# Kernel tuning notes

Measured on AMD Instinct MI355X. Metric: run time of the kernel, lower is better.

Reference implementation:

```python
import jax, jax.numpy as jnp
import numpy as np

N_NODES = 50000
N_EDGES = 1600000
N_GRAPHS = 64
F_IN = 256
H = 1024
EPS = 1e-5


def setup_inputs() -> dict:
    key = jax.random.key(0)
    ks = jax.random.split(key, 6)
    x = jax.random.normal(ks[0], (N_NODES, F_IN), dtype=jnp.float32)
    edge_index = jax.random.randint(ks[1], (2, N_EDGES), 0, N_NODES, dtype=jnp.int32)
    batch = jnp.sort(jax.random.randint(ks[2], (N_NODES,), 0, N_GRAPHS, dtype=jnp.int32))
    # Glorot-ish init for GCN weights
    W0 = jax.random.normal(ks[3], (F_IN, H), dtype=jnp.float32) * (1.0 / np.sqrt(F_IN))
    b0 = jnp.zeros((H,), dtype=jnp.float32)
    Ws = jax.random.normal(ks[4], (3, H, H), dtype=jnp.float32) * (1.0 / np.sqrt(H))
    bs = jnp.zeros((3, H), dtype=jnp.float32)
    gammas = jnp.ones((4, H), dtype=jnp.float32)
    betas = jnp.zeros((4, H), dtype=jnp.float32)
    return {"x": x, "edge_index": edge_index, "batch": batch,
            "W0": W0, "b0": b0, "Ws": Ws, "bs": bs,
            "gammas": gammas, "betas": betas}


def _gcn_norm(edge_index, n_nodes):
    # Add self-loops (PyG GCNConv default), compute symmetric normalization.
    loops = jnp.arange(n_nodes, dtype=edge_index.dtype)
    row = jnp.concatenate([edge_index[0], loops])  # sources
    col = jnp.concatenate([edge_index[1], loops])  # targets (aggregation index)
    ones = jnp.ones(row.shape[0], dtype=jnp.float32)
    deg = jax.ops.segment_sum(ones, col, num_segments=n_nodes)
    dinv = jnp.where(deg > 0, jax.lax.rsqrt(deg), 0.0)
    norm = dinv[row] * dinv[col]  # [E + N]
    return row, col, norm


def _layer(h, W, b, gamma, beta, row, col, norm):
    ht = h @ W                                           # [N, H] GEMM
    msg = ht[row] * norm[:, None]                        # gather + scale
    agg = jax.ops.segment_sum(msg, col, num_segments=N_NODES) + b
    mu = jnp.mean(agg, axis=-1, keepdims=True)
    var = jnp.mean(jnp.square(agg - mu), axis=-1, keepdims=True)
    hn = (agg - mu) * jax.lax.rsqrt(var + EPS) * gamma + beta
    return jax.nn.relu(hn)


def reference(x, edge_index, batch, W0, b0, Ws, bs, gammas, betas):
    row, col, norm = _gcn_norm(edge_index, N_NODES)
    h = _layer(x, W0, b0, gammas[0], betas[0], row, col, norm)
    for i in range(3):
        h = _layer(h, Ws[i], bs[i], gammas[i + 1], betas[i + 1], row, col, norm)
    # scatter_mean over batch (graph-level pooling)
    sums = jax.ops.segment_sum(h, batch, num_segments=N_GRAPHS)
    cnt = jax.ops.segment_sum(jnp.ones((N_NODES,), jnp.float32), batch, num_segments=N_GRAPHS)
    return sums / jnp.maximum(cnt, 1.0)[:, None]
```

## Files before the change

### kernel.cpp

```cpp
#include <hip/hip_runtime.h>
#include <hip/hip_bf16.h>
#include <stdint.h>

#define NN 50000
#define NE 1600000
#define NG 64
#define FIN 256
#define HD 1024
#define EPSV 1e-5f

typedef __bf16 bf16;
typedef float f32x4 __attribute__((ext_vector_type(4)));
typedef int i32x4 __attribute__((ext_vector_type(4)));

typedef const __attribute__((address_space(1))) void* gptr_as1;
typedef __attribute__((address_space(3))) void* lptr_as3;

__device__ __forceinline__ void load_g2l_16(const void* g, const void* l) {
  __builtin_amdgcn_global_load_lds((gptr_as1)(uintptr_t)g,
                                   (lptr_as3)(uint32_t)(uintptr_t)l, 16, 0, 0);
}

__global__ void hist_kernel(const int* __restrict__ col, int* __restrict__ cnt, int E) {
  int e = blockIdx.x * 256 + threadIdx.x;
  if (e < E) atomicAdd(&cnt[col[e]], 1);
}

__global__ void scan_partial_kernel(const int* __restrict__ cnt, int* __restrict__ partial, int n) {
  __shared__ int red[4];
  int i = blockIdx.x * 256 + threadIdx.x;
  int v = (i < n) ? cnt[i] : 0;
  #pragma unroll
  for (int off = 32; off; off >>= 1) v += __shfl_down(v, off, 64);
  if ((threadIdx.x & 63) == 0) red[threadIdx.x >> 6] = v;
  __syncthreads();
  if (threadIdx.x == 0) partial[blockIdx.x] = red[0] + red[1] + red[2] + red[3];
}

__global__ void scan_scan_kernel(int* __restrict__ partial, int nb) {
  __shared__ int s[256];
  int t = threadIdx.x;
  int v = (t < nb) ? partial[t] : 0;
  s[t] = v;
  __syncthreads();
  for (int off = 1; off < 256; off <<= 1) {
    int x = (t >= off) ? s[t - off] : 0;
    __syncthreads();
    s[t] += x;
    __syncthreads();
  }
  if (t < nb) partial[t] = s[t] - v;
}

__global__ void scan_final_kernel(const int* __restrict__ cnt, const int* __restrict__ partial,
                                  int* __restrict__ row_ptr, float* __restrict__ dinv,
                                  int n, int E) {
  __shared__ int s[256];
  int t = threadIdx.x;
  int i = blockIdx.x * 256 + t;
  int v = (i < n) ? cnt[i] : 0;
  s[t] = v;
  __syncthreads();
  for (int off = 1; off < 256; off <<= 1) {
    int x = (t >= off) ? s[t - off] : 0;
    __syncthreads();
    s[t] += x;
    __syncthreads();
  }
  if (i < n) {
    row_ptr[i] = partial[blockIdx.x] + s[t] - v;
    dinv[i] = rsqrtf((float)(v + 1));
  }
  if (i == 0) row_ptr[n] = E;
}

__global__ void scatter_kernel(const int* __restrict__ rowi, const int* __restrict__ coli,
                               const int* __restrict__ row_ptr, int* __restrict__ fill,
                               const float* __restrict__ dinv,
                               int2* __restrict__ csr_sw, int E) {
  int e = blockIdx.x * 256 + threadIdx.x;
  if (e >= E) return;
  int s = rowi[e], d = coli[e];
  int pos = row_ptr[d] + atomicAdd(&fill[d], 1);
  int2 p;
  p.x = s;
  p.y = __float_as_int(dinv[s] * dinv[d]);
  csr_sw[pos] = p;
}

__global__ __launch_bounds__(256) void quant_x_kernel(const float* __restrict__ x,
                                                      uint8_t* __restrict__ X8,
                                                      float* __restrict__ xscale) {
  int row = blockIdx.x * 4 + (threadIdx.x >> 6);
  int t = threadIdx.x & 63;
  float4 v = ((const float4*)(x + (size_t)row * FIN))[t];
  float m = fmaxf(fmaxf(fabsf(v.x), fabsf(v.y)), fmaxf(fabsf(v.z), fabsf(v.w)));
  #pragma unroll
  for (int off = 32; off; off >>= 1) m = fmaxf(m, __shfl_xor(m, off, 64));
  float inv = (m > 0.f) ? 127.0f / m : 0.f;
  int q0 = min(127, max(-127, __float2int_rn(v.x * inv))) + 128;
  int q1 = min(127, max(-127, __float2int_rn(v.y * inv))) + 128;
  int q2 = min(127, max(-127, __float2int_rn(v.z * inv))) + 128;
  int q3 = min(127, max(-127, __float2int_rn(v.w * inv))) + 128;
  uint32_t p = ((uint32_t)q0) | ((uint32_t)q1 << 8) |
               ((uint32_t)q2 << 16) | ((uint32_t)q3 << 24);
  ((uint32_t*)X8)[(size_t)row * 64 + t] = p;
  if (t == 0) xscale[row] = (m > 0.f) ? m / 127.0f : 0.f;
}

__global__ __launch_bounds__(256) void agg0_kernel(
    const uint8_t* __restrict__ X8, const float* __restrict__ xscale,
    const int* __restrict__ row_ptr, const int2* __restrict__ csr_sw,
    const float* __restrict__ dinv,
    int8_t* __restrict__ AX8, float* __restrict__ axscale) {
  const int node = blockIdx.x * 4 + (threadIdx.x >> 6);
  const int t = threadIdx.x & 63;

  float acc[4] = {};
  float sw = 0.f;

  float dn = dinv[node];
  float wself = dn * dn * xscale[node];
  {
    uint32_t d = ((const uint32_t*)X8)[(size_t)node * 64 + t];
    sw += wself;
    acc[0] += wself * (float)(d & 0xffu);
    acc[1] += wself * (float)((d >> 8) & 0xffu);
    acc[2] += wself * (float)((d >> 16) & 0xffu);
    acc[3] += wself * (float)(d >> 24);
  }

  int e = row_ptr[node];
  const int e1 = row_ptr[node + 1];
  for (; e + 4 <= e1; e += 4) {
    int2 p0 = csr_sw[e], p1 = csr_sw[e + 1], p2 = csr_sw[e + 2], p3 = csr_sw[e + 3];
    float w0 = __int_as_float(p0.y) * xscale[p0.x];
    float w1 = __int_as_float(p1.y) * xscale[p1.x];
    float w2 = __int_as_float(p2.y) * xscale[p2.x];
    float w3 = __int_as_float(p3.y) * xscale[p3.x];
    uint32_t d0 = ((const uint32_t*)X8)[(size_t)p0.x * 64 + t];
    uint32_t d1 = ((const uint32_t*)X8)[(size_t)p1.x * 64 + t];
    uint32_t d2 = ((const uint32_t*)X8)[(size_t)p2.x * 64 + t];
    uint32_t d3 = ((const uint32_t*)X8)[(size_t)p3.x * 64 + t];
    sw += w0 + w1 + w2 + w3;
    acc[0] += w0 * (float)(d0 & 0xffu) + w1 * (float)(d1 & 0xffu)
            + w2 * (float)(d2 & 0xffu) + w3 * (float)(d3 & 0xffu);
    acc[1] += w0 * (float)((d0 >> 8) & 0xffu) + w1 * (float)((d1 >> 8) & 0xffu)
            + w2 * (float)((d2 >> 8) & 0xffu) + w3 * (float)((d3 >> 8) & 0xffu);
    acc[2] += w0 * (float)((d0 >> 16) & 0xffu) + w1 * (float)((d1 >> 16) & 0xffu)
            + w2 * (float)((d2 >> 16) & 0xffu) + w3 * (float)((d3 >> 16) & 0xffu);
    acc[3] += w0 * (float)(d0 >> 24) + w1 * (float)(d1 >> 24)
            + w2 * (float)(d2 >> 24) + w3 * (float)(d3 >> 24);
  }
  for (; e < e1; e++) {
    int2 p = csr_sw[e];
    float w = __int_as_float(p.y) * xscale[p.x];
    uint32_t d = ((const uint32_t*)X8)[(size_t)p.x * 64 + t];
    sw += w;
    acc[0] += w * (float)(d & 0xffu);
    acc[1] += w * (float)((d >> 8) & 0xffu);
    acc[2] += w * (float)((d >> 16) & 0xffu);
    acc[3] += w * (float)(d >> 24);
  }

  float c = 128.0f * sw;
  #pragma unroll
  for (int j = 0; j < 4; j++) acc[j] -= c;

  float rm = fmaxf(fmaxf(fabsf(acc[0]), fabsf(acc[1])), fmaxf(fabsf(acc[2]), fabsf(acc[3])));
  #pragma unroll
  for (int off = 32; off; off >>= 1) rm = fmaxf(rm, __shfl_xor(rm, off, 64));
  float qinv = (rm > 0.f) ? 127.0f / rm : 0.f;
  int q0 = min(127, max(-127, __float2int_rn(acc[0] * qinv)));
  int q1 = min(127, max(-127, __float2int_rn(acc[1] * qinv)));
  int q2 = min(127, max(-127, __float2int_rn(acc[2] * qinv)));
  int q3 = min(127, max(-127, __float2int_rn(acc[3] * qinv)));
  uint32_t p = ((uint32_t)(q0 & 0xff)) | ((uint32_t)(q1 & 0xff) << 8) |
               ((uint32_t)(q2 & 0xff) << 16) | ((uint32_t)(q3 & 0xff) << 24);
  ((uint32_t*)AX8)[(size_t)node * 64 + t] = p;
  if (t == 0) axscale[node] = (rm > 0.f) ? rm / 127.0f : 0.f;
}

__global__ __launch_bounds__(256) void ln0_kernel(
    const uint8_t* __restrict__ htu8, const float* __restrict__ scales,
    const float* __restrict__ bias, const float* __restrict__ gamma,
    const float* __restrict__ beta,
    int8_t* __restrict__ hq, float* __restrict__ hscale) {
  const int g = threadIdx.x >> 7;
  const int node = blockIdx.x * 2 + g;
  const int tt = threadIdx.x & 127;
  const int cbL = tt >> 4;
  const int wid = threadIdx.x >> 6;
  __shared__ float red[4];

  float sc = scales[(size_t)node * 8 + cbL];
  uint2 dd = ((const uint2*)(htu8 + (size_t)node * HD))[tt];
  float acc[8];
  acc[0] = sc * ((float)(dd.x & 0xffu) - 128.f);
  acc[1] = sc * ((float)((dd.x >> 8) & 0xffu) - 128.f);
  acc[2] = sc * ((float)((dd.x >> 16) & 0xffu) - 128.f);
  acc[3] = sc * ((float)(dd.x >> 24) - 128.f);
  acc[4] = sc * ((float)(dd.y & 0xffu) - 128.f);
  acc[5] = sc * ((float)((dd.y >> 8) & 0xffu) - 128.f);
  acc[6] = sc * ((float)((dd.y >> 16) & 0xffu) - 128.f);
  acc[7] = sc * ((float)(dd.y >> 24) - 128.f);

  const float4* bias2 = (const float4*)bias;
  float4 ba = bias2[tt * 2], bb = bias2[tt * 2 + 1];
  acc[0] += ba.x; acc[1] += ba.y; acc[2] += ba.z; acc[3] += ba.w;
  acc[4] += bb.x; acc[5] += bb.y; acc[6] += bb.z; acc[7] += bb.w;

  float s = 0.f;
  #pragma unroll
  for (int j = 0; j < 8; j++) s += acc[j];
  #pragma unroll
  for (int off = 32; off; off >>= 1) s += __shfl_down(s, off, 64);
  if ((threadIdx.x & 63) == 0) red[wid] = s;
  __syncthreads();
  float mean = (red[g * 2] + red[g * 2 + 1]) * (1.0f / HD);
  __syncthreads();

  float d[8], s2 = 0.f;
  #pragma unroll
  for (int j = 0; j < 8; j++) { d[j] = acc[j] - mean; s2 += d[j] * d[j]; }
  #pragma unroll
  for (int off = 32; off; off >>= 1) s2 += __shfl_down(s2, off, 64);
  if ((threadIdx.x & 63) == 0) red[wid] = s2;
  __syncthreads();
  float var = (red[g * 2] + red[g * 2 + 1]) * (1.0f / HD);
  float rstd = rsqrtf(var + EPSV);

  const float4* gam2 = (const float4*)gamma;
  const float4* bet2 = (const float4*)beta;
  float4 g0 = gam2[tt * 2], g1 = gam2[tt * 2 + 1];
  float4 be0 = bet2[tt * 2], be1 = bet2[tt * 2 + 1];
  float gv[8] = {g0.x, g0.y, g0.z, g0.w, g1.x, g1.y, g1.z, g1.w};
  float bv[8] = {be0.x, be0.y, be0.z, be0.w, be1.x, be1.y, be1.z, be1.w};
  float o[8];
  float rmax = 0.f;
  #pragma unroll
  for (int j = 0; j < 8; j++) {
    o[j] = fmaxf(d[j] * rstd * gv[j] + bv[j], 0.0f);
    rmax = fmaxf(rmax, o[j]);
  }

  __syncthreads();
  #pragma unroll
  for (int off = 32; off; off >>= 1) rmax = fmaxf(rmax, __shfl_xor(rmax, off, 64));
  if ((threadIdx.x & 63) == 0) red[wid] = rmax;
  __syncthreads();
  float rm = fmaxf(red[g * 2], red[g * 2 + 1]);
  float qinv = (rm > 0.f) ? 127.0f / rm : 0.f;
  int q[8];
  #pragma unroll
  for (int j = 0; j < 8; j++) q[j] = min(127, __float2int_rn(o[j] * qinv));
  uint32_t p0 = ((uint32_t)q[0]) | ((uint32_t)q[1] << 8) | ((uint32_t)q[2] << 16) | ((uint32_t)q[3] << 24);
  uint32_t p1 = ((uint32_t)q[4]) | ((uint32_t)q[5] << 8) | ((uint32_t)q[6] << 16) | ((uint32_t)q[7] << 24);
  uint2 pk; pk.x = p0; pk.y = p1;
  ((uint2*)(hq + (size_t)node * HD))[tt] = pk;
  if (tt == 0) hscale[node] = (rm > 0.f) ? rm / 127.0f : 0.f;
}

__device__ __forceinline__ const float* layer_W(const float* W0, const float* Ws, int L) {
  return (L == 0) ? W0 : Ws + (size_t)(L - 1) * HD * HD;
}

__global__ void wamax_full_kernel(const float* __restrict__ W0, const float* __restrict__ Ws,
                                  float* __restrict__ colmaxf, float* __restrict__ wscale) {
  __shared__ float lds[8][32];
  int L = blockIdx.y;
  int K = (L == 0) ? FIN : HD;
  const float* W = layer_W(W0, Ws, L);
  int n = blockIdx.x * 32 + threadIdx.x;
  float m = 0.f;
  for (int k = threadIdx.y; k < K; k += 8)
    m = fmaxf(m, fabsf(W[(size_t)k * HD + n]));
  lds[threadIdx.y][threadIdx.x] = m;
  __syncthreads();
  if (threadIdx.y == 0) {
    #pragma unroll
    for (int i = 1; i < 8; i++) m = fmaxf(m, lds[i][threadIdx.x]);
    colmaxf[L * HD + n] = m;
    wscale[L * HD + n] = (m > 0.f) ? m / 127.0f : 0.f;
  }
}

__global__ void transpose_wq8_all_kernel(const float* __restrict__ W0,
                                         const float* __restrict__ Ws,
                                         const float* __restrict__ colmaxf,
                                         int8_t* __restrict__ Wt8_all) {
  __shared__ float tile[32][33];
  int L = blockIdx.z;
  int K = (L == 0) ? FIN : HD;
  int k0 = blockIdx.y * 32;
  if (k0 >= K) return;
  const float* W = layer_W(W0, Ws, L);
  int8_t* Wt8 = Wt8_all + ((L == 0) ? 0 : (size_t)FIN * HD + (size_t)(L - 1) * HD * HD);
  int n0 = blockIdx.x * 32;
  int tx = threadIdx.x, ty = threadIdx.y;
  #pragma unroll
  for (int i = ty; i < 32; i += 8) tile[i][tx] = W[(size_t)(k0 + i) * HD + n0 + tx];
  __syncthreads();
  #pragma unroll
  for (int i = ty; i < 32; i += 8) {
    float cm = colmaxf[L * HD + n0 + i];
    float inv = (cm > 0.f) ? 127.0f / cm : 0.f;
    int q = min(127, max(-127, __float2int_rn(tile[tx][i] * inv)));
    Wt8[(size_t)(n0 + i) * K + k0 + tx] = (int8_t)q;
  }
}

__global__ __launch_bounds__(256, 4) void gemm_i8_q8_kernel(
    const int8_t* __restrict__ A8, const float* __restrict__ hscale,
    const int8_t* __restrict__ Wt8, const float* __restrict__ wscale,
    uint8_t* __restrict__ C8, float* __restrict__ scales, int M, int K) {
  __shared__ __align__(16) int8_t As[2][128 * 64];
  __shared__ __align__(16) int8_t Bs[2][128 * 64];
  __shared__ float smax[2][128];
  const int tid = threadIdx.x;
  const int w = tid >> 6, l = tid & 63;

  const int nwg = gridDim.x;
  const int o = blockIdx.x;
  const int lid = (o & 7) * (nwg >> 3) + (o >> 3);
  const int m0 = (lid >> 3) * 128, n0 = (lid & 7) * 128;
  const int cb = lid & 7;
  const int wr = w >> 1, wc = w & 1;

  i32x4 acc[4][4] = {};

  const int r0 = tid >> 2;
  const int c16 = (tid & 3) * 16;
  int ar0 = m0 + r0;       if (ar0 >= M) ar0 = M - 1;
  int ar1 = m0 + r0 + 64;  if (ar1 >= M) ar1 = M - 1;
  const int8_t* a0 = A8 + (size_t)ar0 * K + c16;
  const int8_t* a1 = A8 + (size_t)ar1 * K + c16;
  const int8_t* b0 = Wt8 + (size_t)(n0 + r0) * K + c16;
  const int8_t* b1 = Wt8 + (size_t)(n0 + r0 + 64) * K + c16;

  const int mrow = l & 15;
  const int kch = (l >> 4) * 16;

  auto stage = [&](int b, int k) {
    int8_t* asw = &As[b][w * 1024];
    int8_t* bsw = &Bs[b][w * 1024];
    load_g2l_16(a0 + k, asw);
    load_g2l_16(a1 + k, asw + 4096);
    load_g2l_16(b0 + k, bsw);
    load_g2l_16(b1 + k, bsw + 4096);
  };

  const int nit = K >> 6;
  stage(0, 0);
  __syncthreads();

  int cur = 0;
  for (int t = 0; t < nit; ++t) {
    if (t + 1 < nit) stage(cur ^ 1, (t + 1) << 6);
    i32x4 af[4], bf_[4];
    #pragma unroll
    for (int m = 0; m < 4; m++)
      af[m] = *(const i32x4*)&As[cur][(wr * 64 + m * 16 + mrow) * 64 + kch];
    #pragma unroll
    for (int n = 0; n < 4; n++)
      bf_[n] = *(const i32x4*)&Bs[cur][(wc * 64 + n * 16 + mrow) * 64 + kch];
    #pragma unroll
    for (int m = 0; m < 4; m++)
      #pragma unroll
      for (int n = 0; n < 4; n++)
        acc[m][n] = __builtin_amdgcn_mfma_i32_16x16x64_i8(af[m], bf_[n], acc[m][n], 0, 0, 0);
    __syncthreads();
    cur ^= 1;
  }

  float wsv[4];
  #pragma unroll
  for (int n = 0; n < 4; n++) wsv[n] = wscale[n0 + wc * 64 + n * 16 + (l & 15)];

  #pragma unroll
  for (int m = 0; m < 4; m++) {
    #pragma unroll
    for (int r = 0; r < 4; r++) {
      int rl = wr * 64 + m * 16 + (l >> 4) * 4 + r;
      int grow = m0 + rl; if (grow >= M) grow = M - 1;
      float v = 0.f;
      #pragma unroll
      for (int n = 0; n < 4; n++)
        v = fmaxf(v, fabsf((float)acc[m][n][r] * wsv[n]));
      v *= hscale[grow];
      #pragma unroll
      for (int mask = 1; mask < 16; mask <<= 1) v = fmaxf(v, __shfl_xor(v, mask, 64));
      if ((l & 15) == 0) smax[wc][rl] = v;
    }
  }
  __syncthreads();

  #pragma unroll
  for (int m = 0; m < 4; m++) {
    #pragma unroll
    for (int r = 0; r < 4; r++) {
      int rl = wr * 64 + m * 16 + (l >> 4) * 4 + r;
      int grow = m0 + rl;
      float mx = fmaxf(smax[0][rl], smax[1][rl]);
      float inv = (mx > 0.f) ? 127.0f / mx : 0.f;
      if (grow < M) {
        float hs = hscale[grow];
        if (wc == 0 && (l & 15) == 0)
          scales[(size_t)grow * 8 + cb] = (mx > 0.f) ? mx / 127.0f : 0.f;
        #pragma unroll
        for (int n = 0; n < 4; n++) {
          int gcol = n0 + wc * 64 + n * 16 + (l & 15);
          int u = __float2int_rn((float)acc[m][n][r] * hs * wsv[n] * inv) + 128;
          C8[(size_t)grow * HD + gcol] = (uint8_t)u;
        }
      }
    }
  }
}

__global__ __launch_bounds__(256) void agg_ln_u8_kernel(
    const uint8_t* __restrict__ htu8, const float* __restrict__ scales,
    const int* __restrict__ row_ptr, const int2* __restrict__ csr_sw,
    const float* __restrict__ dinv, const float* __restrict__ bias,
    const float* __restrict__ gamma, const float* __restrict__ beta,
    int8_t* __restrict__ hq, float* __restrict__ hscale) {
  const int node = blockIdx.x * 4 + (threadIdx.x >> 6);
  const int l = threadIdx.x & 63;
  const int cbL = l >> 3;

  float acc[16] = {};
  float sw = 0.f;

  auto ACC = [&](float w, const uint4& dd) {
    sw += w;
    const uint32_t dw[4] = {dd.x, dd.y, dd.z, dd.w};
    #pragma unroll
    for (int c = 0; c < 4; c++) {
      acc[4 * c + 0] += w * (float)(dw[c] & 0xffu);
      acc[4 * c + 1] += w * (float)((dw[c] >> 8) & 0xffu);
      acc[4 * c + 2] += w * (float)((dw[c] >> 16) & 0xffu);
      acc[4 * c + 3] += w * (float)(dw[c] >> 24);
    }
  };

  float dn = dinv[node];
  float wself = dn * dn * scales[(size_t)node * 8 + cbL];
  ACC(wself, ((const uint4*)(htu8 + (size_t)node * HD))[l]);

  int e = row_ptr[node];
  const int e1 = row_ptr[node + 1];
  for (; e + 4 <= e1; e += 4) {
    int2 p0 = csr_sw[e], p1 = csr_sw[e + 1], p2 = csr_sw[e + 2], p3 = csr_sw[e + 3];
    float w0 = __int_as_float(p0.y) * scales[(size_t)p0.x * 8 + cbL];
    float w1 = __int_as_float(p1.y) * scales[(size_t)p1.x * 8 + cbL];
    float w2 = __int_as_float(p2.y) * scales[(size_t)p2.x * 8 + cbL];
    float w3 = __int_as_float(p3.y) * scales[(size_t)p3.x * 8 + cbL];
    uint4 d0 = ((const uint4*)(htu8 + (size_t)p0.x * HD))[l];
    uint4 d1 = ((const uint4*)(htu8 + (size_t)p1.x * HD))[l];
    uint4 d2 = ((const uint4*)(htu8 + (size_t)p2.x * HD))[l];
    uint4 d3 = ((const uint4*)(htu8 + (size_t)p3.x * HD))[l];
    ACC(w0, d0);
    ACC(w1, d1);
    ACC(w2, d2);
    ACC(w3, d3);
  }
  for (; e < e1; e++) {
    int2 p = csr_sw[e];
    float wgt = __int_as_float(p.y) * scales[(size_t)p.x * 8 + cbL];
    ACC(wgt, ((const uint4*)(htu8 + (size_t)p.x * HD))[l]);
  }

  const float4* bias4 = (const float4*)bias;
  float c128 = 128.0f * sw;
  #pragma unroll
  for (int c = 0; c < 4; c++) {
    float4 bb = bias4[l * 4 + c];
    acc[4 * c + 0] += bb.x - c128;
    acc[4 * c + 1] += bb.y - c128;
    acc[4 * c + 2] += bb.z - c128;
    acc[4 * c + 3] += bb.w - c128;
  }

  float s = 0.f;
  #pragma unroll
  for (int j = 0; j < 16; j++) s += acc[j];
  #pragma unroll
  for (int off = 32; off; off >>= 1) s += __shfl_xor(s, off, 64);
  float mean = s * (1.0f / HD);

  float d[16], s2 = 0.f;
  #pragma unroll
  for (int j = 0; j < 16; j++) { d[j] = acc[j] - mean; s2 += d[j] * d[j]; }
  #pragma unroll
  for (int off = 32; off; off >>= 1) s2 += __shfl_xor(s2, off, 64);
  float rstd = rsqrtf(s2 * (1.0f / HD) + EPSV);

  const float4* gam4 = (const float4*)gamma;
  const float4* bet4 = (const float4*)beta;
  float o[16];
  float rmax = 0.f;
  #pragma unroll
  for (int c = 0; c < 4; c++) {
    float4 gg = gam4[l * 4 + c];
    float4 be = bet4[l * 4 + c];
    float gv[4] = {gg.x, gg.y, gg.z, gg.w};
    float bv[4] = {be.x, be.y, be.z, be.w};
    #pragma unroll
    for (int j = 0; j < 4; j++) {
      float v = fmaxf(d[4 * c + j] * rstd * gv[j] + bv[j], 0.0f);
      o[4 * c + j] = v;
      rmax = fmaxf(rmax, v);
    }
  }
  #pragma unroll
  for (int off = 32; off; off >>= 1) rmax = fmaxf(rmax, __shfl_xor(rmax, off, 64));
  float qinv = (rmax > 0.f) ? 127.0f / rmax : 0.f;

  uint32_t pw[4];
  #pragma unroll
  for (int c = 0; c < 4; c++) {
    int q0 = min(127, __float2int_rn(o[4 * c + 0] * qinv));
    int q1 = min(127, __float2int_rn(o[4 * c + 1] * qinv));
    int q2 = min(127, __float2int_rn(o[4 * c + 2] * qinv));
    int q3 = min(127, __float2int_rn(o[4 * c + 3] * qinv));
    pw[c] = ((uint32_t)q0) | ((uint32_t)q1 << 8) | ((uint32_t)q2 << 16) | ((uint32_t)q3 << 24);
  }
  uint4 pk; pk.x = pw[0]; pk.y = pw[1]; pk.z = pw[2]; pk.w = pw[3];
  ((uint4*)(hq + (size_t)node * HD))[l] = pk;
  if (l == 0) hscale[node] = (rmax > 0.f) ? rmax / 127.0f : 0.f;
}

__global__ void starts_kernel(const int* __restrict__ batch, int* __restrict__ start,
                              int n, int ngraph) {
  int g = blockIdx.x * blockDim.x + threadIdx.x;
  if (g > ngraph) return;
  int lo = 0, hi = n;
  while (lo < hi) {
    int mid = (lo + hi) >> 1;
    if (batch[mid] < g) lo = mid + 1; else hi = mid;
  }
  start[g] = lo;
}

#define POOL_CHUNKS 8
__global__ void pool_partial_kernel(const int8_t* __restrict__ hq,
                                    const float* __restrict__ hscale,
                                    const int* __restrict__ start,
                                    float* __restrict__ out) {
  int g = blockIdx.y, c = blockIdx.x;
  int t = threadIdx.x;
  int s0 = start[g], s1 = start[g + 1];
  int len = s1 - s0;
  int per = (len + POOL_CHUNKS - 1) / POOL_CHUNKS;
  int a = s0 + c * per;
  int b = min(a + per, s1);
  if (a >= b) return;
  f32x4 acc = {0.f, 0.f, 0.f, 0.f};
  for (int n = a; n < b; n++) {
    float hs = hscale[n];
    uint32_t d = ((const uint32_t*)(hq + (size_t)n * HD))[t];
    acc[0] += hs * (float)(d & 0xffu);
    acc[1] += hs * (float)((d >> 8) & 0xffu);
    acc[2] += hs * (float)((d >> 16) & 0xffu);
    acc[3] += hs * (float)(d >> 24);
  }
  float* o = out + (size_t)g * HD + t * 4;
  atomicAdd(o + 0, acc[0]);
  atomicAdd(o + 1, acc[1]);
  atomicAdd(o + 2, acc[2]);
  atomicAdd(o + 3, acc[3]);
}

__global__ void pool_div_kernel(float* __restrict__ out, const int* __restrict__ start) {
  int i = blockIdx.x * 256 + threadIdx.x;
  if (i >= NG * HD) return;
  int g = i >> 10;
  float c = (float)max(start[g + 1] - start[g], 1);
  out[i] = out[i] / c;
}

extern "C" void kernel_launch(void* const* d_in, const int* in_sizes, int n_in,
                              void* d_out, int out_size, void* d_ws, size_t ws_size,
                              hipStream_t stream) {
  const float* x      = (const float*)d_in[0];
  const int*   eidx   = (const int*)d_in[1];
  const int*   batch  = (const int*)d_in[2];
  const float* W0     = (const float*)d_in[3];
  const float* b0     = (const float*)d_in[4];
  const float* Ws     = (const float*)d_in[5];
  const float* bs     = (const float*)d_in[6];
  const float* gammas = (const float*)d_in[7];
  const float* betas  = (const float*)d_in[8];
  float* out = (float*)d_out;

  const int* erow = eidx;
  const int* ecol = eidx + NE;

  char* ws = (char*)d_ws;
  size_t off = 0;
  auto alloc = [&](size_t bytes) {
    void* p = ws + off;
    off = (off + bytes + 255) & ~(size_t)255;
    return p;
  };
  int*     cnt     = (int*)alloc((size_t)NN * 4);
  int*     row_ptr = (int*)alloc((size_t)(NN + 1) * 4);
  int*     fill    = (int*)alloc((size_t)NN * 4);
  int*     partial = (int*)alloc(256 * 4);
  float*   dinv    = (float*)alloc((size_t)NN * 4);
  int2*    csr_sw  = (int2*)alloc((size_t)NE * 8);
  int8_t*  Wt8     = (int8_t*)alloc((size_t)FIN * HD + 3 * (size_t)HD * HD);
  int8_t*  A8      = (int8_t*)alloc((size_t)NN * HD);
  uint8_t* ht8     = (uint8_t*)alloc((size_t)NN * HD);
  float*   scales  = (float*)alloc((size_t)NN * 8 * 4);
  uint8_t* X8      = (uint8_t*)alloc((size_t)NN * FIN);
  int8_t*  AX8     = (int8_t*)alloc((size_t)NN * FIN);
  float*   xscale  = (float*)alloc((size_t)NN * 4);
  float*   axscale = (float*)alloc((size_t)NN * 4);
  int*     gstart  = (int*)alloc(65 * 4);

  float* wscale  = (float*)cnt;
  float* colmaxf = (float*)cnt + 4096;
  float* hscale  = (float*)fill;

  hipMemsetAsync(cnt, 0, (size_t)NN * 4, stream);
  hipMemsetAsync(fill, 0, (size_t)NN * 4, stream);
  hipMemsetAsync(out, 0, (size_t)NG * HD * 4, stream);

  hist_kernel<<<(NE + 255) / 256, 256, 0, stream>>>(ecol, cnt, NE);
  int nb = (NN + 255) / 256;
  scan_partial_kernel<<<nb, 256, 0, stream>>>(cnt, partial, NN);
  scan_scan_kernel<<<1, 256, 0, stream>>>(partial, nb);
  scan_final_kernel<<<nb, 256, 0, stream>>>(cnt, partial, row_ptr, dinv, NN, NE);
  scatter_kernel<<<(NE + 255) / 256, 256, 0, stream>>>(erow, ecol, row_ptr, fill, dinv,
                                                       csr_sw, NE);
  starts_kernel<<<1, 128, 0, stream>>>(batch, gstart, NN, NG);

  quant_x_kernel<<<NN / 4, 256, 0, stream>>>(x, X8, xscale);

  wamax_full_kernel<<<dim3(HD / 32, 4), dim3(32, 8), 0, stream>>>(W0, Ws, colmaxf, wscale);
  transpose_wq8_all_kernel<<<dim3(HD / 32, HD / 32, 4), dim3(32, 8), 0, stream>>>(
      W0, Ws, colmaxf, Wt8);

  const int nmt = (NN + 127) / 128;

  agg0_kernel<<<NN / 4, 256, 0, stream>>>(X8, xscale, row_ptr, csr_sw, dinv, AX8, axscale);
  gemm_i8_q8_kernel<<<nmt * 8, 256, 0, stream>>>(AX8, axscale, Wt8, wscale,
                                                 ht8, scales, NN, FIN);
  ln0_kernel<<<NN / 2, 256, 0, stream>>>(ht8, scales, b0, gammas, betas, A8, hscale);

  for (int L = 1; L < 4; L++) {
    const int8_t* WtL = Wt8 + (size_t)FIN * HD + (size_t)(L - 1) * HD * HD;
    const float* bias = bs + (size_t)(L - 1) * HD;
    gemm_i8_q8_kernel<<<nmt * 8, 256, 0, stream>>>(A8, hscale, WtL, wscale + L * HD,
                                                   ht8, scales, NN, HD);
    agg_ln_u8_kernel<<<NN / 4, 256, 0, stream>>>(ht8, scales, row_ptr, csr_sw,
                                                 dinv, bias, gammas + (size_t)L * HD,
                                                 betas + (size_t)L * HD, A8, hscale);
  }

  pool_partial_kernel<<<dim3(POOL_CHUNKS, NG), 256, 0, stream>>>(A8, hscale, gstart, out);
  pool_div_kernel<<<(NG * HD + 255) / 256, 256, 0, stream>>>(out, gstart);
}
```

Before: 1.412 ms.

## Split aggregation into column-chunked kernel followed by separate layernorm pass

Replaces the fused aggregate+layernorm kernel, which used one wavefront per node over all 1024 columns, with a kernel that assigns 8 threads per node per 128-column chunk. The chunk index is taken from the low bits of blockIdx.x, so the concurrently running blocks gather the same 128-byte slice of neighbor rows and get better cache locality on the random gathers. The aggregated result is requantized to uint8 with per-chunk scales, and the existing ln0 kernel then applies bias, layernorm and ReLU. This adds an extra write and read of an N×1024 byte buffer, an extra launch per layer, and a second quantization step that may cost accuracy.

```diff
diff --git a/kernel.cpp b/kernel.cpp
--- a/kernel.cpp
+++ b/kernel.cpp
@@ -181,6 +181,85 @@
   if (t == 0) axscale[node] = (rm > 0.f) ? rm / 127.0f : 0.f;
 }
 
+__global__ __launch_bounds__(256) void agg_chunk_kernel(
+    const uint8_t* __restrict__ htu8, const float* __restrict__ scales,
+    const int* __restrict__ row_ptr, const int2* __restrict__ csr_sw,
+    const float* __restrict__ dinv,
+    uint8_t* __restrict__ agg8, float* __restrict__ scales2) {
+  const int chunk = blockIdx.x & 7;
+  const int node = (blockIdx.x >> 3) * 32 + (threadIdx.x >> 3);
+  if (node >= NN) return;
+  const int sl = threadIdx.x & 7;
+  const int coff = chunk * 128 + sl * 16;
+
+  float acc[16] = {};
+  float sw = 0.f;
+
+  auto ACC = [&](float w, const uint4& dd) {
+    sw += w;
+    const uint32_t dw[4] = {dd.x, dd.y, dd.z, dd.w};
+    #pragma unroll
+    for (int c = 0; c < 4; c++) {
+      acc[4 * c + 0] += w * (float)(dw[c] & 0xffu);
+      acc[4 * c + 1] += w * (float)((dw[c] >> 8) & 0xffu);
+      acc[4 * c + 2] += w * (float)((dw[c] >> 16) & 0xffu);
+      acc[4 * c + 3] += w * (float)(dw[c] >> 24);
+    }
+  };
+
+  float dn = dinv[node];
+  float wself = dn * dn * scales[(size_t)node * 8 + chunk];
+  ACC(wself, *(const uint4*)(htu8 + (size_t)node * HD + coff));
+
+  int e = row_ptr[node];
+  const int e1 = row_ptr[node + 1];
+  for (; e + 4 <= e1; e += 4) {
+    int2 p0 = csr_sw[e], p1 = csr_sw[e + 1], p2 = csr_sw[e + 2], p3 = csr_sw[e + 3];
+    float w0 = __int_as_float(p0.y) * scales[(size_t)p0.x * 8 + chunk];
+    float w1 = __int_as_float(p1.y) * scales[(size_t)p1.x * 8 + chunk];
+    float w2 = __int_as_float(p2.y) * scales[(size_t)p2.x * 8 + chunk];
+    float w3 = __int_as_float(p3.y) * scales[(size_t)p3.x * 8 + chunk];
+    uint4 d0 = *(const uint4*)(htu8 + (size_t)p0.x * HD + coff);
+    uint4 d1 = *(const uint4*)(htu8 + (size_t)p1.x * HD + coff);
+    uint4 d2 = *(const uint4*)(htu8 + (size_t)p2.x * HD + coff);
+    uint4 d3 = *(const uint4*)(htu8 + (size_t)p3.x * HD + coff);
+    ACC(w0, d0);
+    ACC(w1, d1);
+    ACC(w2, d2);
+    ACC(w3, d3);
+  }
+  for (; e < e1; e++) {
+    int2 p = csr_sw[e];
+    float wgt = __int_as_float(p.y) * scales[(size_t)p.x * 8 + chunk];
+    ACC(wgt, *(const uint4*)(htu8 + (size_t)p.x * HD + coff));
+  }
+
+  float c128 = 128.0f * sw;
+  #pragma unroll
+  for (int j = 0; j < 16; j++) acc[j] -= c128;
+
+  float rm = 0.f;
+  #pragma unroll
+  for (int j = 0; j < 16; j++) rm = fmaxf(rm, fabsf(acc[j]));
+  rm = fmaxf(rm, __shfl_xor(rm, 1, 64));
+  rm = fmaxf(rm, __shfl_xor(rm, 2, 64));
+  rm = fmaxf(rm, __shfl_xor(rm, 4, 64));
+  float qinv = (rm > 0.f) ? 127.0f / rm : 0.f;
+
+  uint32_t pw[4];
+  #pragma unroll
+  for (int c = 0; c < 4; c++) {
+    int q0 = min(127, max(-127, __float2int_rn(acc[4 * c + 0] * qinv))) + 128;
+    int q1 = min(127, max(-127, __float2int_rn(acc[4 * c + 1] * qinv))) + 128;
+    int q2 = min(127, max(-127, __float2int_rn(acc[4 * c + 2] * qinv))) + 128;
+    int q3 = min(127, max(-127, __float2int_rn(acc[4 * c + 3] * qinv))) + 128;
+    pw[c] = ((uint32_t)q0) | ((uint32_t)q1 << 8) | ((uint32_t)q2 << 16) | ((uint32_t)q3 << 24);
+  }
+  uint4 pk; pk.x = pw[0]; pk.y = pw[1]; pk.z = pw[2]; pk.w = pw[3];
+  *(uint4*)(agg8 + (size_t)node * HD + coff) = pk;
+  if (sl == 0) scales2[(size_t)node * 8 + chunk] = (rm > 0.f) ? rm / 127.0f : 0.f;
+}
+
 __global__ __launch_bounds__(256) void ln0_kernel(
     const uint8_t* __restrict__ htu8, const float* __restrict__ scales,
     const float* __restrict__ bias, const float* __restrict__ gamma,
@@ -416,118 +495,6 @@
       }
     }
   }
-}
-
-__global__ __launch_bounds__(256) void agg_ln_u8_kernel(
-    const uint8_t* __restrict__ htu8, const float* __restrict__ scales,
-    const int* __restrict__ row_ptr, const int2* __restrict__ csr_sw,
-    const float* __restrict__ dinv, const float* __restrict__ bias,
-    const float* __restrict__ gamma, const float* __restrict__ beta,
-    int8_t* __restrict__ hq, float* __restrict__ hscale) {
-  const int node = blockIdx.x * 4 + (threadIdx.x >> 6);
-  const int l = threadIdx.x & 63;
-  const int cbL = l >> 3;
-
-  float acc[16] = {};
-  float sw = 0.f;
-
-  auto ACC = [&](float w, const uint4& dd) {
-    sw += w;
-    const uint32_t dw[4] = {dd.x, dd.y, dd.z, dd.w};
-    #pragma unroll
-    for (int c = 0; c < 4; c++) {
-      acc[4 * c + 0] += w * (float)(dw[c] & 0xffu);
-      acc[4 * c + 1] += w * (float)((dw[c] >> 8) & 0xffu);
-      acc[4 * c + 2] += w * (float)((dw[c] >> 16) & 0xffu);
-      acc[4 * c + 3] += w * (float)(dw[c] >> 24);
-    }
-  };
-
-  float dn = dinv[node];
-  float wself = dn * dn * scales[(size_t)node * 8 + cbL];
-  ACC(wself, ((const uint4*)(htu8 + (size_t)node * HD))[l]);
-
-  int e = row_ptr[node];
-  const int e1 = row_ptr[node + 1];
-  for (; e + 4 <= e1; e += 4) {
-    int2 p0 = csr_sw[e], p1 = csr_sw[e + 1], p2 = csr_sw[e + 2], p3 = csr_sw[e + 3];
-    float w0 = __int_as_float(p0.y) * scales[(size_t)p0.x * 8 + cbL];
-    float w1 = __int_as_float(p1.y) * scales[(size_t)p1.x * 8 + cbL];
-    float w2 = __int_as_float(p2.y) * scales[(size_t)p2.x * 8 + cbL];
-    float w3 = __int_as_float(p3.y) * scales[(size_t)p3.x * 8 + cbL];
-    uint4 d0 = ((const uint4*)(htu8 + (size_t)p0.x * HD))[l];
-    uint4 d1 = ((const uint4*)(htu8 + (size_t)p1.x * HD))[l];
-    uint4 d2 = ((const uint4*)(htu8 + (size_t)p2.x * HD))[l];
-    uint4 d3 = ((const uint4*)(htu8 + (size_t)p3.x * HD))[l];
-    ACC(w0, d0);
-    ACC(w1, d1);
-    ACC(w2, d2);
-    ACC(w3, d3);
-  }
-  for (; e < e1; e++) {
-    int2 p = csr_sw[e];
-    float wgt = __int_as_float(p.y) * scales[(size_t)p.x * 8 + cbL];
-    ACC(wgt, ((const uint4*)(htu8 + (size_t)p.x * HD))[l]);
-  }
-
-  const float4* bias4 = (const float4*)bias;
-  float c128 = 128.0f * sw;
-  #pragma unroll
-  for (int c = 0; c < 4; c++) {
-    float4 bb = bias4[l * 4 + c];
-    acc[4 * c + 0] += bb.x - c128;
-    acc[4 * c + 1] += bb.y - c128;
-    acc[4 * c + 2] += bb.z - c128;
-    acc[4 * c + 3] += bb.w - c128;
-  }
-
-  float s = 0.f;
-  #pragma unroll
-  for (int j = 0; j < 16; j++) s += acc[j];
-  #pragma unroll
-  for (int off = 32; off; off >>= 1) s += __shfl_xor(s, off, 64);
-  float mean = s * (1.0f / HD);
-
-  float d[16], s2 = 0.f;
-  #pragma unroll
-  for (int j = 0; j < 16; j++) { d[j] = acc[j] - mean; s2 += d[j] * d[j]; }
-  #pragma unroll
-  for (int off = 32; off; off >>= 1) s2 += __shfl_xor(s2, off, 64);
-  float rstd = rsqrtf(s2 * (1.0f / HD) + EPSV);
-
-  const float4* gam4 = (const float4*)gamma;
-  const float4* bet4 = (const float4*)beta;
-  float o[16];
-  float rmax = 0.f;
-  #pragma unroll
-  for (int c = 0; c < 4; c++) {
-    float4 gg = gam4[l * 4 + c];
-    float4 be = bet4[l * 4 + c];
-    float gv[4] = {gg.x, gg.y, gg.z, gg.w};
-    float bv[4] = {be.x, be.y, be.z, be.w};
-    #pragma unroll
-    for (int j = 0; j < 4; j++) {
-      float v = fmaxf(d[4 * c + j] * rstd * gv[j] + bv[j], 0.0f);
-      o[4 * c + j] = v;
-      rmax = fmaxf(rmax, v);
-    }
-  }
-  #pragma unroll
-  for (int off = 32; off; off >>= 1) rmax = fmaxf(rmax, __shfl_xor(rmax, off, 64));
-  float qinv = (rmax > 0.f) ? 127.0f / rmax : 0.f;
-
-  uint32_t pw[4];
-  #pragma unroll
-  for (int c = 0; c < 4; c++) {
-    int q0 = min(127, __float2int_rn(o[4 * c + 0] * qinv));
-    int q1 = min(127, __float2int_rn(o[4 * c + 1] * qinv));
-    int q2 = min(127, __float2int_rn(o[4 * c + 2] * qinv));
-    int q3 = min(127, __float2int_rn(o[4 * c + 3] * qinv));
-    pw[c] = ((uint32_t)q0) | ((uint32_t)q1 << 8) | ((uint32_t)q2 << 16) | ((uint32_t)q3 << 24);
-  }
-  uint4 pk; pk.x = pw[0]; pk.y = pw[1]; pk.z = pw[2]; pk.w = pw[3];
-  ((uint4*)(hq + (size_t)node * HD))[l] = pk;
-  if (l == 0) hscale[node] = (rmax > 0.f) ? rmax / 127.0f : 0.f;
 }
 
 __global__ void starts_kernel(const int* __restrict__ batch, int* __restrict__ start,
@@ -613,6 +580,8 @@
   int8_t*  A8      = (int8_t*)alloc((size_t)NN * HD);
   uint8_t* ht8     = (uint8_t*)alloc((size_t)NN * HD);
   float*   scales  = (float*)alloc((size_t)NN * 8 * 4);
+  uint8_t* agg8    = (uint8_t*)alloc((size_t)NN * HD);
+  float*   scales2 = (float*)alloc((size_t)NN * 8 * 4);
   uint8_t* X8      = (uint8_t*)alloc((size_t)NN * FIN);
   int8_t*  AX8     = (int8_t*)alloc((size_t)NN * FIN);
   float*   xscale  = (float*)alloc((size_t)NN * 4);
@@ -643,6 +612,7 @@
       W0, Ws, colmaxf, Wt8);
 
   const int nmt = (NN + 127) / 128;
+  const int nagg = ((NN + 31) / 32) * 8;
 
   agg0_kernel<<<NN / 4, 256, 0, stream>>>(X8, xscale, row_ptr, csr_sw, dinv, AX8, axscale);
   gemm_i8_q8_kernel<<<nmt * 8, 256, 0, stream>>>(AX8, axscale, Wt8, wscale,
@@ -654,9 +624,10 @@
     const float* bias = bs + (size_t)(L - 1) * HD;
     gemm_i8_q8_kernel<<<nmt * 8, 256, 0, stream>>>(A8, hscale, WtL, wscale + L * HD,
                                                    ht8, scales, NN, HD);
-    agg_ln_u8_kernel<<<NN / 4, 256, 0, stream>>>(ht8, scales, row_ptr, csr_sw,
-                                                 dinv, bias, gammas + (size_t)L * HD,
-                                                 betas + (size_t)L * HD, A8, hscale);
+    agg_chunk_kernel<<<nagg, 256, 0, stream>>>(ht8, scales, row_ptr, csr_sw, dinv,
+                                               agg8, scales2);
+    ln0_kernel<<<NN / 2, 256, 0, stream>>>(agg8, scales2, bias, gammas + (size_t)L * HD,
+                                           betas + (size_t)L * HD, A8, hscale);
   }
 
   pool_partial_kernel<<<dim3(POOL_CHUNKS, NG), 256, 0, stream>>>(A8, hscale, gstart, out);
```

After: 1.574 ms. 1.11x slower.
